# Performance work log

Hardware: AMD Instinct MI355X
Metric: run time of the kernel (lower is better)

Reference implementation:

```python
import jax, jax.numpy as jnp
import numpy as np

B, S, D = 4, 2048, 512
H = 8
DH = D // H  # depth per head = 64
SCALE = 1.0 / np.sqrt(np.float32(D))  # NOTE: original divides by sqrt(feature_size), not sqrt(depth)
EPS = 1e-5


def setup_inputs() -> dict:
    key = jax.random.key(0)
    ks = jax.random.split(key, 10)
    std = 1.0 / np.sqrt(D)
    inp = {
        "x": jax.random.normal(ks[0], (B, S, D), dtype=jnp.float32),
        "w_q": jax.random.uniform(ks[1], (D, D), jnp.float32, -std, std),
        "b_q": jax.random.uniform(ks[2], (D,), jnp.float32, -std, std),
        "w_k": jax.random.uniform(ks[3], (D, D), jnp.float32, -std, std),
        "b_k": jax.random.uniform(ks[4], (D,), jnp.float32, -std, std),
        "w_v": jax.random.uniform(ks[5], (D, D), jnp.float32, -std, std),
        "b_v": jax.random.uniform(ks[6], (D,), jnp.float32, -std, std),
        "w_o": jax.random.uniform(ks[7], (D, D), jnp.float32, -std, std),
        "b_o": jax.random.uniform(ks[8], (D,), jnp.float32, -std, std),
        "ln_gamma": jnp.ones((D,), jnp.float32),
        "ln_beta": jnp.zeros((D,), jnp.float32),
    }
    return inp


def _split_heads(t):
    # [B, S, D] -> [B, H, S, DH]
    return t.reshape(B, S, H, DH).transpose(0, 2, 1, 3)


def reference(x, w_q, b_q, w_k, b_k, w_v, b_v, w_o, b_o, ln_gamma, ln_beta):
    q = _split_heads(x @ w_q.T + b_q)
    k = _split_heads(x @ w_k.T + b_k)
    v = _split_heads(x @ w_v.T + b_v)
    # scores: [B, H, S, S], scaled by 1/sqrt(feature_size) per the original
    scores = jnp.einsum("bhqd,bhkd->bhqk", q, k) * SCALE
    alpha = jax.nn.softmax(scores, axis=-1)
    context = jnp.einsum("bhqk,bhkd->bhqd", alpha, v)
    context = context.transpose(0, 2, 1, 3).reshape(B, S, D)
    out = context @ w_o.T + b_o
    # residual + LayerNorm
    y = out + x
    mu = jnp.mean(y, axis=-1, keepdims=True)
    var = jnp.mean(jnp.square(y - mu), axis=-1, keepdims=True)
    y = (y - mu) * jax.lax.rsqrt(var + EPS)
    return y * ln_gamma + ln_beta
```

## Files before the change

### kernel.cpp

```cpp
#include <hip/hip_runtime.h>
#include <hip/hip_bf16.h>
#include <math.h>

#define BB 4
#define SS 2048
#define DD 512
#define HH 8
#define DHH 64
#define MROWS (BB*SS)

constexpr float SCALE  = 0.044194173824159216f;
constexpr float QSCALE = (float)(0.044194173824159216 * 1.4426950408889634);
constexpr float LN_EPS = 1e-5f;

typedef __attribute__((ext_vector_type(8)))  short bf16x8;
typedef __attribute__((ext_vector_type(4)))  float f32x4;
typedef __attribute__((ext_vector_type(16))) float f32x16;

__device__ __forceinline__ ushort f2bf(float f) {
    __hip_bfloat16 h = __float2bfloat16(f);
    ushort u; __builtin_memcpy(&u, &h, 2);
    return u;
}

__device__ __forceinline__ float exp2_hw(float x) {
#if __has_builtin(__builtin_amdgcn_exp2f)
    return __builtin_amdgcn_exp2f(x);
#else
    return exp2f(x);
#endif
}

__device__ __forceinline__ unsigned cvt_pk_bf16(float lo, float hi) {
    unsigned r;
    asm("v_cvt_pk_bf16_f32 %0, %1, %2" : "=v"(r) : "v"(lo), "v"(hi));
    return r;
}
__device__ __forceinline__ void plane_swap(unsigned &a, unsigned &b) {
    asm("v_permlane32_swap_b32 %0, %1" : "+v"(a), "+v"(b));
}
__device__ __forceinline__ bf16x8 pack4(unsigned a0, unsigned a1, unsigned b0, unsigned b1) {
    union { unsigned u[4]; bf16x8 v; } x;
    x.u[0] = a0; x.u[1] = a1; x.u[2] = b0; x.u[3] = b1;
    return x.v;
}

__device__ __forceinline__ void gload16(const void* gsrc, void* lds_dst) {
    __builtin_amdgcn_global_load_lds(
        (const __attribute__((address_space(1))) unsigned int*)gsrc,
        (__attribute__((address_space(3))) unsigned int*)lds_dst,
        16, 0, 0);
}

__global__ __launch_bounds__(256) void cast_kernel(
    const float* __restrict__ x,
    const float* __restrict__ wq, const float* __restrict__ wk,
    const float* __restrict__ wv, const float* __restrict__ wo,
    const float* __restrict__ bq, const float* __restrict__ bk,
    const float* __restrict__ bv,
    ushort* __restrict__ xb, ushort* __restrict__ wb, float* __restrict__ biasc)
{
    const int gid = blockIdx.x * 256 + threadIdx.x;
    if (gid < 1536) {
        float v = gid < 512 ? bq[gid] * QSCALE
                : gid < 1024 ? bk[gid - 512] : bv[gid - 1024];
        biasc[gid] = v;
    }
    const int NX4 = (MROWS * DD) / 4;
    const int NW4 = (DD * DD) / 4;
    const int total = NX4 + 4 * NW4;
    for (int i = gid; i < total; i += gridDim.x * 256) {
        float4 v; ushort4 o;
        if (i < NX4) {
            v = ((const float4*)x)[i];
            o.x = f2bf(v.x); o.y = f2bf(v.y); o.z = f2bf(v.z); o.w = f2bf(v.w);
            ((ushort4*)xb)[i] = o;
        } else {
            int j = i - NX4;
            int which = j >> 16;
            int off = j & 65535;
            const float4* src = which == 0 ? (const float4*)wq
                              : which == 1 ? (const float4*)wk
                              : which == 2 ? (const float4*)wv : (const float4*)wo;
            v = src[off];
            float scl = which == 0 ? QSCALE : 1.0f;
            o.x = f2bf(v.x * scl); o.y = f2bf(v.y * scl);
            o.z = f2bf(v.z * scl); o.w = f2bf(v.w * scl);
            ((ushort4*)wb)[j] = o;
        }
    }
}

__device__ __forceinline__ void stage_tile(const ushort* __restrict__ g, int k0,
                                           ushort* lbuf, int t)
{
    #pragma unroll
    for (int i = 0; i < 4; ++i) {
        int cc = i * 256 + t;
        int row = cc >> 3, slot = cc & 7;
        gload16(g + row * DD + k0 + ((slot ^ (row & 7)) << 3), lbuf + cc * 8);
    }
}

__device__ __forceinline__ void mma_step(const ushort* Abuf, const ushort* Bbuf,
                                         int wr, int wc, int c, int g,
                                         f32x4 (&acc)[4][4])
{
    bf16x8 af[2][4], bf[2][4];
    #pragma unroll
    for (int kc = 0; kc < 2; ++kc) {
        int sw = ((kc * 4 + g) ^ (c & 7)) << 4;
        #pragma unroll
        for (int mi = 0; mi < 4; ++mi)
            af[kc][mi] = *(const bf16x8*)((const char*)Abuf + (wr*64 + mi*16 + c)*128 + sw);
        #pragma unroll
        for (int ni = 0; ni < 4; ++ni)
            bf[kc][ni] = *(const bf16x8*)((const char*)Bbuf + (wc*64 + ni*16 + c)*128 + sw);
    }
    __builtin_amdgcn_s_setprio(1);
    #pragma unroll
    for (int kc = 0; kc < 2; ++kc)
        #pragma unroll
        for (int mi = 0; mi < 4; ++mi)
            #pragma unroll
            for (int ni = 0; ni < 4; ++ni)
                acc[mi][ni] = __builtin_amdgcn_mfma_f32_16x16x32_bf16(
                    af[kc][mi], bf[kc][ni], acc[mi][ni], 0, 0, 0);
    __builtin_amdgcn_s_setprio(0);
}

__global__ __launch_bounds__(256) void qkv_mm(
    const ushort* __restrict__ xb, const ushort* __restrict__ wb,
    const float* __restrict__ biasc,
    ushort* __restrict__ Qb, ushort* __restrict__ Kb, ushort* __restrict__ Vtb)
{
    __shared__ ushort Abuf[128*64];
    __shared__ ushort Bbuf[128*64];
    const int t = threadIdx.x, w = t >> 6, lane = t & 63;
    const int wr = w >> 1, wc = w & 1, c = lane & 15, g = lane >> 4;
    const int nblk = blockIdx.x, mblk = blockIdx.y;

    const ushort* Ag = xb + (size_t)mblk * 128 * DD;
    const ushort* Bg = wb + (size_t)nblk * 128 * DD;

    f32x4 acc[4][4] = {};

    for (int k0 = 0; k0 < DD; k0 += 64) {
        stage_tile(Ag, k0, Abuf, t);
        stage_tile(Bg, k0, Bbuf, t);
        __syncthreads();
        mma_step(Abuf, Bbuf, wr, wc, c, g, acc);
        __syncthreads();
    }

    const int n0 = nblk * 128;
    const int proj = n0 >> 9;
    #pragma unroll
    for (int mi = 0; mi < 4; ++mi) {
        int m = mblk*128 + wr*64 + mi*16 + g*4;
        int bi = m >> 11, s = m & 2047;
        #pragma unroll
        for (int ni = 0; ni < 4; ++ni) {
            int ng = n0 + wc*64 + ni*16 + c;
            float bias = biasc[ng];
            int col = ng & 511, h = col >> 6, d = col & 63;
            if (proj == 2) {
                ushort4 o = { f2bf(acc[mi][ni][0] + bias), f2bf(acc[mi][ni][1] + bias),
                              f2bf(acc[mi][ni][2] + bias), f2bf(acc[mi][ni][3] + bias) };
                *(ushort4*)&Vtb[(((size_t)bi*HH + h)*DHH + d)*SS + s] = o;
            } else {
                ushort* outb = proj == 0 ? Qb : Kb;
                #pragma unroll
                for (int rg = 0; rg < 4; ++rg) {
                    outb[(((size_t)bi*HH + h)*SS + (s + rg))*DHH + d] = f2bf(acc[mi][ni][rg] + bias);
                }
            }
        }
    }
}

__global__ __launch_bounds__(256) void oproj_mm(
    const ushort* __restrict__ ctx, const ushort* __restrict__ wob,
    const float* __restrict__ bo, const float* __restrict__ resid,
    float* __restrict__ out)
{
    __shared__ ushort Abuf[128*64];
    __shared__ ushort Bbuf[128*64];
    const int t = threadIdx.x, w = t >> 6, lane = t & 63;
    const int wr = w >> 1, wc = w & 1, c = lane & 15, g = lane >> 4;
    const int nblk = blockIdx.x, mblk = blockIdx.y;

    const ushort* Ag = ctx + (size_t)mblk * 128 * DD;
    const ushort* Bg = wob + (size_t)nblk * 128 * DD;

    f32x4 acc[4][4] = {};

    for (int k0 = 0; k0 < DD; k0 += 64) {
        stage_tile(Ag, k0, Abuf, t);
        stage_tile(Bg, k0, Bbuf, t);
        __syncthreads();
        mma_step(Abuf, Bbuf, wr, wc, c, g, acc);
        __syncthreads();
    }

    #pragma unroll
    for (int mi = 0; mi < 4; ++mi) {
        int m = mblk*128 + wr*64 + mi*16 + g*4;
        #pragma unroll
        for (int ni = 0; ni < 4; ++ni) {
            int ng = nblk*128 + wc*64 + ni*16 + c;
            float bias = bo[ng];
            #pragma unroll
            for (int rg = 0; rg < 4; ++rg) {
                int mm = m + rg;
                out[(size_t)mm*DD + ng] = acc[mi][ni][rg] + bias + resid[(size_t)mm*DD + ng];
            }
        }
    }
}

__global__ __launch_bounds__(256) void attn_kernel(
    const ushort* __restrict__ Q, const ushort* __restrict__ K,
    const ushort* __restrict__ Vt, ushort* __restrict__ ctx)
{
    __shared__ ushort Ks[2][64*64];
    __shared__ ushort Vts[2][64*64];

    const int t = threadIdx.x;
    const int w = t >> 6, l = t & 63;
    const int ln31 = l & 31, hi = l >> 5, l7 = l & 7;

    const int id  = blockIdx.x;
    const int swz = (id & 7) * 64 + (id >> 3);
    const int qt = swz & 15;
    const int h  = (swz >> 4) & 7;
    const int b  = swz >> 7;
    const size_t bh = (size_t)b * HH + h;
    const int q0 = qt*128 + w*32;

    const ushort* Qp = Q + (bh * SS + (size_t)q0 + ln31) * DHH;
    bf16x8 qf[4];
    #pragma unroll
    for (int s = 0; s < 4; ++s)
        qf[s] = *(const bf16x8*)&Qp[s*16 + hi*8];

    bf16x8 onesf;
    {
        union { short s[8]; bf16x8 v; } u;
        #pragma unroll
        for (int i = 0; i < 8; ++i) u.s[i] = (short)0x3F80;
        onesf = u.v;
    }

    const int r = t >> 3, sl = t & 7;
    const int swsl = (sl ^ (r & 7)) << 3;
    const ushort* Kbase  = K  + bh * SS * DHH;
    const ushort* Vtbase = Vt + bh * DHH * SS;

#define ATTN_STAGE(kvi, bi_) do {                                          \
        const ushort* kp_ = Kbase  + (size_t)(kvi) * 64 * DHH;             \
        const ushort* vp_ = Vtbase + (kvi) * 64;                           \
        _Pragma("unroll")                                                  \
        for (int i_ = 0; i_ < 2; ++i_) {                                   \
            gload16(kp_ + (32*i_ + r)*DHH + swsl,                          \
                    &Ks[bi_][(32*i_ + r)*64 + sl*8]);                      \
            gload16(vp_ + (size_t)(32*i_ + r)*SS + swsl,                   \
                    &Vts[bi_][(32*i_ + r)*64 + sl*8]);                     \
        }                                                                  \
    } while (0)

    f32x16 ot[2] = {};
    f32x16 zacc  = {};

    ATTN_STAGE(0, 0);

    for (int kv = 0; kv < SS/64; ++kv) {
        const int cur = kv & 1;
        __syncthreads();
        if (kv + 1 < SS/64) ATTN_STAGE(kv + 1, cur ^ 1);

        const ushort* Kc = Ks[cur];
        const ushort* Vc = Vts[cur];

        f32x16 st[2];
        __builtin_amdgcn_s_setprio(1);
        #pragma unroll
        for (int kt = 0; kt < 2; ++kt) {
            f32x16 z = {};
            #pragma unroll
            for (int s = 0; s < 4; ++s) {
                bf16x8 kf = *(const bf16x8*)((const char*)Kc
                            + (kt*32 + ln31)*128 + (((2*s + hi) ^ l7) << 4));
                z = __builtin_amdgcn_mfma_f32_32x32x16_bf16(kf, qf[s], z, 0, 0, 0);
            }
            st[kt] = z;
        }
        __builtin_amdgcn_s_setprio(0);

        #pragma unroll
        for (int kt = 0; kt < 2; ++kt)
            #pragma unroll
            for (int i = 0; i < 16; ++i)
                st[kt][i] = exp2_hw(st[kt][i]);

        unsigned dk[2][4][2];
        #pragma unroll
        for (int kt = 0; kt < 2; ++kt)
            #pragma unroll
            for (int rb = 0; rb < 4; ++rb) {
                dk[kt][rb][0] = cvt_pk_bf16(st[kt][4*rb+0], st[kt][4*rb+1]);
                dk[kt][rb][1] = cvt_pk_bf16(st[kt][4*rb+2], st[kt][4*rb+3]);
            }
        bf16x8 pb[2][2];
        #pragma unroll
        for (int kt = 0; kt < 2; ++kt)
            #pragma unroll
            for (int s2 = 0; s2 < 2; ++s2) {
                unsigned a0 = dk[kt][2*s2][0], b0 = dk[kt][2*s2+1][0];
                unsigned a1 = dk[kt][2*s2][1], b1 = dk[kt][2*s2+1][1];
                plane_swap(a0, b0);
                plane_swap(a1, b1);
                pb[kt][s2] = pack4(a0, a1, b0, b1);
            }

        __builtin_amdgcn_s_setprio(1);
        #pragma unroll
        for (int kt = 0; kt < 2; ++kt)
            #pragma unroll
            for (int s2 = 0; s2 < 2; ++s2) {
                #pragma unroll
                for (int dt = 0; dt < 2; ++dt) {
                    bf16x8 vf = *(const bf16x8*)((const char*)Vc
                                + (dt*32 + ln31)*128 + (((kt*4 + 2*s2 + hi) ^ l7) << 4));
                    ot[dt] = __builtin_amdgcn_mfma_f32_32x32x16_bf16(vf, pb[kt][s2], ot[dt], 0, 0, 0);
                }
                zacc = __builtin_amdgcn_mfma_f32_32x32x16_bf16(onesf, pb[kt][s2], zacc, 0, 0, 0);
            }
        __builtin_amdgcn_s_setprio(0);
    }
#undef ATTN_STAGE

    const float rl = 1.f / zacc[0];
    ushort* outp = ctx + ((size_t)b*SS + q0 + ln31) * DD + h*DHH;
    #pragma unroll
    for (int dt = 0; dt < 2; ++dt)
        #pragma unroll
        for (int rb = 0; rb < 4; ++rb) {
            ushort4 o = { f2bf(ot[dt][4*rb+0]*rl), f2bf(ot[dt][4*rb+1]*rl),
                          f2bf(ot[dt][4*rb+2]*rl), f2bf(ot[dt][4*rb+3]*rl) };
            *(ushort4*)&outp[dt*32 + rb*8 + hi*4] = o;
        }
}

__global__ __launch_bounds__(256) void ln_kernel(
    const float* __restrict__ y, const float* __restrict__ gamma,
    const float* __restrict__ beta, float* __restrict__ out)
{
    const int row = blockIdx.x;
    const int t = threadIdx.x;
    const float* yr = y + (size_t)row * DD;

    float2 v = *(const float2*)&yr[t*2];
    float s  = v.x + v.y;
    float sq = v.x*v.x + v.y*v.y;
    #pragma unroll
    for (int off = 1; off < 64; off <<= 1) {
        s  += __shfl_xor(s,  off);
        sq += __shfl_xor(sq, off);
    }
    __shared__ float ss[4], ssq[4];
    int wv = t >> 6;
    if ((t & 63) == 0) { ss[wv] = s; ssq[wv] = sq; }
    __syncthreads();
    s  = ss[0] + ss[1] + ss[2] + ss[3];
    sq = ssq[0] + ssq[1] + ssq[2] + ssq[3];

    float mean = s * (1.0f / DD);
    float var  = sq * (1.0f / DD) - mean * mean;
    float rstd = rsqrtf(var + LN_EPS);

    float2 g  = *(const float2*)&gamma[t*2];
    float2 be = *(const float2*)&beta[t*2];
    float2 o;
    o.x = (v.x - mean) * rstd * g.x + be.x;
    o.y = (v.y - mean) * rstd * g.y + be.y;
    *(float2*)&out[(size_t)row * DD + t*2] = o;
}

extern "C" void kernel_launch(void* const* d_in, const int* in_sizes, int n_in,
                              void* d_out, int out_size, void* d_ws, size_t ws_size,
                              hipStream_t stream)
{
    const float* x     = (const float*)d_in[0];
    const float* wq    = (const float*)d_in[1];
    const float* bq    = (const float*)d_in[2];
    const float* wk    = (const float*)d_in[3];
    const float* bk    = (const float*)d_in[4];
    const float* wv    = (const float*)d_in[5];
    const float* bv    = (const float*)d_in[6];
    const float* wo    = (const float*)d_in[7];
    const float* bo    = (const float*)d_in[8];
    const float* gamma = (const float*)d_in[9];
    const float* beta  = (const float*)d_in[10];

    char* wsb = (char*)d_ws;
    const size_t MB = 1u << 20;
    ushort* xb    = (ushort*)(wsb + 0*MB);
    ushort* wb    = (ushort*)(wsb + 8*MB);
    float*  biasc = (float* )(wsb + 10*MB);
    ushort* Qb    = (ushort*)(wsb + 11*MB);
    ushort* Kb    = (ushort*)(wsb + 19*MB);
    ushort* Vtb   = (ushort*)(wsb + 27*MB);
    ushort* ctxb  = (ushort*)(wsb + 35*MB);
    float*  ybuf  = (float*)(wsb + 11*MB);

    cast_kernel<<<2048, 256, 0, stream>>>(x, wq, wk, wv, wo, bq, bk, bv,
                                          xb, wb, biasc);
    {
        dim3 grid(12, 64);
        qkv_mm<<<grid, 256, 0, stream>>>(xb, wb, biasc, Qb, Kb, Vtb);
    }
    {
        attn_kernel<<<512, 256, 0, stream>>>(Qb, Kb, Vtb, ctxb);
    }
    {
        dim3 grid(4, 64);
        oproj_mm<<<grid, 256, 0, stream>>>(ctxb, wb + 3*DD*DD, bo, x, ybuf);
    }
    ln_kernel<<<MROWS, 256, 0, stream>>>(ybuf, gamma, beta, (float*)d_out);
}
```

Before: 111.7 us.

## Split KV range across two wave groups in attention and combine via LDS

Doubles the attention block to 512 threads. The two groups of four waves each process half of the KV sequence for the same 128 query rows, using separate double-buffered LDS tiles. At the end the partial outputs and normalizers are summed through LDS and one group writes the result. This halves the serial KV loop per wave and puts more waves on each CU to hide latency. In exchange it doubles LDS use and adds a combine step with extra barriers. The plain summation is only correct because the softmax keeps no running max.

```diff
diff --git a/kernel.cpp b/kernel.cpp
--- a/kernel.cpp
+++ b/kernel.cpp
@@ -219,16 +219,17 @@
     }
 }
 
-__global__ __launch_bounds__(256) void attn_kernel(
+__global__ __launch_bounds__(512) void attn_kernel(
     const ushort* __restrict__ Q, const ushort* __restrict__ K,
     const ushort* __restrict__ Vt, ushort* __restrict__ ctx)
 {
-    __shared__ ushort Ks[2][64*64];
-    __shared__ ushort Vts[2][64*64];
+    __shared__ ushort Ks[2][2][64*64];
+    __shared__ ushort Vts[2][2][64*64];
 
     const int t = threadIdx.x;
     const int w = t >> 6, l = t & 63;
     const int ln31 = l & 31, hi = l >> 5, l7 = l & 7;
+    const int qb = w & 3, kvh = w >> 2;
 
     const int id  = blockIdx.x;
     const int swz = (id & 7) * 64 + (id >> 3);
@@ -236,7 +237,7 @@
     const int h  = (swz >> 4) & 7;
     const int b  = swz >> 7;
     const size_t bh = (size_t)b * HH + h;
-    const int q0 = qt*128 + w*32;
+    const int q0 = qt*128 + qb*32;
 
     const ushort* Qp = Q + (bh * SS + (size_t)q0 + ln31) * DHH;
     bf16x8 qf[4];
@@ -252,20 +253,23 @@
         onesf = u.v;
     }
 
-    const int r = t >> 3, sl = t & 7;
+    const int t2 = t & 255;
+    const int r = t2 >> 3, sl = t2 & 7;
     const int swsl = (sl ^ (r & 7)) << 3;
     const ushort* Kbase  = K  + bh * SS * DHH;
     const ushort* Vtbase = Vt + bh * DHH * SS;
+    const int NT = SS/64/2;
 
 #define ATTN_STAGE(kvi, bi_) do {                                          \
-        const ushort* kp_ = Kbase  + (size_t)(kvi) * 64 * DHH;             \
-        const ushort* vp_ = Vtbase + (kvi) * 64;                           \
+        const int tix_ = kvh*NT + (kvi);                                   \
+        const ushort* kp_ = Kbase  + (size_t)tix_ * 64 * DHH;              \
+        const ushort* vp_ = Vtbase + tix_ * 64;                            \
         _Pragma("unroll")                                                  \
         for (int i_ = 0; i_ < 2; ++i_) {                                   \
             gload16(kp_ + (32*i_ + r)*DHH + swsl,                          \
-                    &Ks[bi_][(32*i_ + r)*64 + sl*8]);                      \
+                    &Ks[kvh][bi_][(32*i_ + r)*64 + sl*8]);                 \
             gload16(vp_ + (size_t)(32*i_ + r)*SS + swsl,                   \
-                    &Vts[bi_][(32*i_ + r)*64 + sl*8]);                     \
+                    &Vts[kvh][bi_][(32*i_ + r)*64 + sl*8]);                \
         }                                                                  \
     } while (0)
 
@@ -274,13 +278,13 @@
 
     ATTN_STAGE(0, 0);
 
-    for (int kv = 0; kv < SS/64; ++kv) {
+    for (int kv = 0; kv < NT; ++kv) {
         const int cur = kv & 1;
         __syncthreads();
-        if (kv + 1 < SS/64) ATTN_STAGE(kv + 1, cur ^ 1);
-
-        const ushort* Kc = Ks[cur];
-        const ushort* Vc = Vts[cur];
+        if (kv + 1 < NT) ATTN_STAGE(kv + 1, cur ^ 1);
+
+        const ushort* Kc = Ks[kvh][cur];
+        const ushort* Vc = Vts[kvh][cur];
 
         f32x16 st[2];
         __builtin_amdgcn_s_setprio(1);
@@ -340,16 +344,29 @@
     }
 #undef ATTN_STAGE
 
-    const float rl = 1.f / zacc[0];
-    ushort* outp = ctx + ((size_t)b*SS + q0 + ln31) * DD + h*DHH;
-    #pragma unroll
-    for (int dt = 0; dt < 2; ++dt)
-        #pragma unroll
-        for (int rb = 0; rb < 4; ++rb) {
-            ushort4 o = { f2bf(ot[dt][4*rb+0]*rl), f2bf(ot[dt][4*rb+1]*rl),
-                          f2bf(ot[dt][4*rb+2]*rl), f2bf(ot[dt][4*rb+3]*rl) };
-            *(ushort4*)&outp[dt*32 + rb*8 + hi*4] = o;
-        }
+    __syncthreads();
+    float* comb = (float*)&Ks[0][0][0];
+    float* p = comb + (size_t)(qb*64 + l) * 33;
+    if (kvh == 0) {
+        #pragma unroll
+        for (int i = 0; i < 16; ++i) { p[i] = ot[0][i]; p[16+i] = ot[1][i]; }
+        p[32] = zacc[0];
+    }
+    __syncthreads();
+    if (kvh == 1) {
+        const float rl = 1.f / (zacc[0] + p[32]);
+        ushort* outp = ctx + ((size_t)b*SS + q0 + ln31) * DD + h*DHH;
+        #pragma unroll
+        for (int dt = 0; dt < 2; ++dt)
+            #pragma unroll
+            for (int rb = 0; rb < 4; ++rb) {
+                ushort4 o = { f2bf((ot[dt][4*rb+0] + p[dt*16+4*rb+0])*rl),
+                              f2bf((ot[dt][4*rb+1] + p[dt*16+4*rb+1])*rl),
+                              f2bf((ot[dt][4*rb+2] + p[dt*16+4*rb+2])*rl),
+                              f2bf((ot[dt][4*rb+3] + p[dt*16+4*rb+3])*rl) };
+                *(ushort4*)&outp[dt*32 + rb*8 + hi*4] = o;
+            }
+    }
 }
 
 __global__ __launch_bounds__(256) void ln_kernel(
@@ -421,7 +438,7 @@
         qkv_mm<<<grid, 256, 0, stream>>>(xb, wb, biasc, Qb, Kb, Vtb);
     }
     {
-        attn_kernel<<<512, 256, 0, stream>>>(Qb, Kb, Vtb, ctxb);
+        attn_kernel<<<512, 512, 0, stream>>>(Qb, Kb, Vtb, ctxb);
     }
     {
         dim3 grid(4, 64);
```

Measured after the change: 105.3 us. 5.7% less time.
